# Optimization experiments

Hardware: AMD Instinct MI355X
Metric: run time of the kernel (lower is better)

Reference implementation:

```python
import jax, jax.numpy as jnp
import numpy as np

N, E, G = 50000, 800000, 512
HD, ED, GD, HID = 128, 64, 64, 128  # h_dim, e_dim, g_dim, hid_dim


def _mlp2(x, W1, b1, W2, b2, last_act):
    # Linear -> ReLU -> Linear (-> optional last activation)
    y = jax.nn.relu(x @ W1 + b1) @ W2 + b2
    return last_act(y) if last_act is not None else y


def setup_inputs() -> dict:
    key = jax.random.key(0)
    ks = list(jax.random.split(key, 24))
    ki = iter(ks)

    def p(shape):
        return (jax.random.normal(next(ki), shape, jnp.float32) * 0.02)

    inp = {
        "h": jax.random.normal(next(ki), (N, HD), jnp.float32),
        "e_index": jax.random.randint(next(ki), (2, E), 0, N),
        "e": jax.random.normal(next(ki), (E, ED), jnp.float32),
        "g": jax.random.normal(next(ki), (G, GD), jnp.float32),
        "batch": jnp.sort(jax.random.randint(next(ki), (N,), 0, G)),
        # fc_m: [2*HD+ED+GD, HID, HID], last_activation=relu
        "W_m1": p((2 * HD + ED + GD, HID)), "b_m1": jnp.zeros((HID,), jnp.float32),
        "W_m2": p((HID, HID)), "b_m2": jnp.zeros((HID,), jnp.float32),
        # fc_m_att: [HID, 1], sigmoid
        "W_ma": p((HID, 1)), "b_ma": jnp.zeros((1,), jnp.float32),
        # fc_e: [HID, ED, ED]
        "W_e1": p((HID, ED)), "b_e1": jnp.zeros((ED,), jnp.float32),
        "W_e2": p((ED, ED)), "b_e2": jnp.zeros((ED,), jnp.float32),
        # fc_h: [HD+HID+GD, HD, HD]
        "W_h1": p((HD + HID + GD, HD)), "b_h1": jnp.zeros((HD,), jnp.float32),
        "W_h2": p((HD, HD)), "b_h2": jnp.zeros((HD,), jnp.float32),
        # fc_h_att: [HD, 1]
        "W_ha": p((HD, 1)), "b_ha": jnp.zeros((1,), jnp.float32),
        # fc_g: [GD+HD, GD, GD]
        "W_g1": p((GD + HD, GD)), "b_g1": jnp.zeros((GD,), jnp.float32),
        "W_g2": p((GD, GD)), "b_g2": jnp.zeros((GD,), jnp.float32),
    }
    return inp


def reference(h, e_index, e, g, batch,
              W_m1, b_m1, W_m2, b_m2, W_ma, b_ma,
              W_e1, b_e1, W_e2, b_e2,
              W_h1, b_h1, W_h2, b_h2, W_ha, b_ha,
              W_g1, b_g1, W_g2, b_g2):
    src, dst = e_index[0], e_index[1]
    e_batch = batch[dst]

    # edge message: concat gathered endpoints + edge feat + gathered global
    m_cat = jnp.concatenate([h[src], h[dst], e, g[e_batch]], axis=1)  # [E, 2HD+ED+GD]
    m = jax.nn.relu(jax.nn.relu(m_cat @ W_m1 + b_m1) @ W_m2 + b_m2)   # [E, HID]
    m_att = jax.nn.sigmoid(m @ W_ma + b_ma)                            # [E, 1]

    e_update = _mlp2(m, W_e1, b_e1, W_e2, b_e2, None)                  # [E, ED]
    e_out = jax.nn.relu(e + e_update)

    m_aggr = jax.ops.segment_sum(m_att * m, dst, num_segments=h.shape[0])  # [N, HID]

    h_cat = jnp.concatenate([h, m_aggr, g[batch]], axis=1)             # [N, HD+HID+GD]
    h_update = _mlp2(h_cat, W_h1, b_h1, W_h2, b_h2, None)
    h_out = jax.nn.relu(h + h_update)                                  # [N, HD]
    h_att = h_out @ W_ha + b_ha                                        # [N, 1]

    h_aggr = jax.ops.segment_sum(h_att * h_out, batch, num_segments=g.shape[0])  # [G, HD]

    g_cat = jnp.concatenate([g, h_aggr], axis=1)                       # [G, GD+HD]
    g_update = _mlp2(g_cat, W_g1, b_g1, W_g2, b_g2, None)
    g_out = jax.nn.relu(g + g_update)

    return (h_out, e_out, g_out)
```

## Files before the change

### kernel.cpp

```cpp
#include <hip/hip_runtime.h>
#include <hip/hip_bf16.h>

#define NN 50000
#define NE 800000
#define NG 512
#define HD 128
#define ED 64
#define GD 64
#define HID 128
#define EB 64

typedef __attribute__((ext_vector_type(8))) short short8;
typedef __attribute__((ext_vector_type(4))) short short4v;
typedef __attribute__((ext_vector_type(2))) float f32x2;
typedef __attribute__((ext_vector_type(4))) float f32x4;

__device__ __forceinline__ short f2bf(float f) {
  union { float f; unsigned u; } v; v.f = f;
  unsigned r = v.u + 0x7fffu + ((v.u >> 16) & 1u);
  return (short)(r >> 16);
}

__device__ __forceinline__ float bf2f(short s) {
  union { unsigned u; float f; } v;
  v.u = ((unsigned)(unsigned short)s) << 16;
  return v.f;
}

__device__ __forceinline__ short8 load_a8(const float* p) {
  const f32x4* q = (const f32x4*)p;
  f32x4 x0 = q[0], x1 = q[1];
  short8 r;
  r[0]=f2bf(x0[0]); r[1]=f2bf(x0[1]); r[2]=f2bf(x0[2]); r[3]=f2bf(x0[3]);
  r[4]=f2bf(x1[0]); r[5]=f2bf(x1[1]); r[6]=f2bf(x1[2]); r[7]=f2bf(x1[3]);
  return r;
}

__device__ __forceinline__ int swz(int row, int col, int rowBytes) {
  int b = row * rowBytes + col * 2;
  b ^= (row & 7) << 4;
  return b >> 1;
}

__global__ void pack_kernel(const float* __restrict__ Wm1, const float* __restrict__ Wm2,
                            const float* __restrict__ We1, const float* __restrict__ We2,
                            const float* __restrict__ Wh1, const float* __restrict__ Wh2,
                            short* __restrict__ out) {
  int gid = blockIdx.x * 256 + threadIdx.x;
  if (gid >= 135168) return;
  const float* W; int Ncol, base, idx;
  if (gid < 49152)       { W = Wm1; Ncol = 128; base = 0;      idx = gid; }
  else if (gid < 65536)  { W = Wm2; Ncol = 128; base = 49152;  idx = gid - 49152; }
  else if (gid < 73728)  { W = We1; Ncol = 64;  base = 65536;  idx = gid - 65536; }
  else if (gid < 77824)  { W = We2; Ncol = 64;  base = 73728;  idx = gid - 73728; }
  else if (gid < 118784) { W = Wh1; Ncol = 128; base = 77824;  idx = gid - 77824; }
  else                   { W = Wh2; Ncol = 128; base = 118784; idx = gid - 118784; }
  int k = idx / Ncol, n = idx % Ncol;
  out[base + (k >> 3) * Ncol * 8 + n * 8 + (k & 7)] = f2bf(W[idx]);
}

__global__ void cast_kernel(const float* __restrict__ h, const float* __restrict__ g,
                            const int* __restrict__ ei,
                            short* __restrict__ h_bf, short* __restrict__ g_bf,
                            int* __restrict__ deg) {
  int gid = blockIdx.x * 256 + threadIdx.x;
  const int H4 = NN * HD / 4;
  const int G4 = NG * GD / 4;
  if (gid < H4) {
    f32x4 v = ((const f32x4*)h)[gid];
    short4v r; r[0]=f2bf(v[0]); r[1]=f2bf(v[1]); r[2]=f2bf(v[2]); r[3]=f2bf(v[3]);
    *(short4v*)(h_bf + gid * 4) = r;
  } else if (gid < H4 + G4) {
    int i = gid - H4;
    f32x4 v = ((const f32x4*)g)[i];
    short4v r; r[0]=f2bf(v[0]); r[1]=f2bf(v[1]); r[2]=f2bf(v[2]); r[3]=f2bf(v[3]);
    *(short4v*)(g_bf + i * 4) = r;
  } else if (gid < H4 + G4 + NE) {
    int i = gid - H4 - G4;
    atomicAdd(&deg[ei[NE + i]], 1);
  }
}

__global__ __launch_bounds__(1024) void scan_kernel(int* __restrict__ deg) {
  __shared__ int psum[1024];
  const int CH = 49;
  int t = threadIdx.x;
  int lo = t * CH, hi = lo + CH; if (hi > NN) hi = NN; if (lo > NN) lo = NN;
  int s = 0;
  for (int i = lo; i < hi; ++i) s += deg[i];
  psum[t] = s;
  __syncthreads();
  for (int d = 1; d < 1024; d <<= 1) {
    int v = (t >= d) ? psum[t - d] : 0;
    __syncthreads();
    psum[t] += v;
    __syncthreads();
  }
  int run = (t == 0) ? 0 : psum[t - 1];
  for (int i = lo; i < hi; ++i) { int v = deg[i]; deg[i] = run; run += v; }
}

__global__ void scatter_kernel(const int* __restrict__ ei, int* __restrict__ off,
                               int* __restrict__ elist) {
  int i = blockIdx.x * 256 + threadIdx.x;
  if (i < NE) {
    int d = ei[NE + i];
    int p = atomicAdd(&off[d], 1);
    elist[p] = i;
  }
}

__global__ __launch_bounds__(256) void edge_kernel(
    const short* __restrict__ h_bf, const int* __restrict__ ei,
    const float* __restrict__ e, const short* __restrict__ g_bf,
    const int* __restrict__ batch, const int* __restrict__ elist,
    const short* __restrict__ pWm1, const float* __restrict__ bm1,
    const short* __restrict__ pWm2, const float* __restrict__ bm2,
    const float* __restrict__ Wma, const float* __restrict__ bma,
    const short* __restrict__ pWe1, const float* __restrict__ be1,
    const short* __restrict__ pWe2, const float* __restrict__ be2,
    float* __restrict__ e_out, float* __restrict__ m_aggr) {
  __shared__ short lds_m[EB * 128];
  __shared__ short bufB[2][4096];
  __shared__ float att_s[EB];
  __shared__ int sdst[EB];
  __shared__ int seid[EB];
  short* ebuf = lds_m;

  const int tid = threadIdx.x;
  const int w = tid >> 6;
  const int lane = tid & 63;
  const int row16 = lane & 15;
  const int quad = lane >> 4;

  int nwg = gridDim.x;
  int q = nwg >> 3, rr = nwg & 7;
  int xcd = blockIdx.x & 7;
  int idx = blockIdx.x >> 3;
  int bid = (xcd < rr ? xcd * (q + 1) : rr * (q + 1) + (xcd - rr) * q) + idx;
  const int eb = bid * EB;

#define STAGE(Wp, c, b) do {                                                  \
    const short* _s = (Wp) + (size_t)(c) * 4096;                              \
    short8 _v0 = *(const short8*)(_s + tid * 8);                              \
    short8 _v1 = *(const short8*)(_s + 2048 + tid * 8);                       \
    *(short8*)&bufB[(b)][tid * 8] = _v0;                                      \
    *(short8*)&bufB[(b)][2048 + tid * 8] = _v1;                               \
  } while (0)

  if (tid < EB) {
    int eid = elist[eb + tid];
    seid[tid] = eid;
    sdst[tid] = ei[NE + eid];
  }

  const int eidr = elist[eb + w * 16 + row16];
  const int dstr = ei[NE + eidr];
  const int srcr = ei[eidr];
  const int gbr = batch[dstr];

  const short* seg0 = h_bf + (size_t)srcr * HD;
  const short* seg1 = h_bf + (size_t)dstr * HD;
  const short* seg3 = g_bf + (size_t)gbr * GD;

  short8 ea0, ea1;
  {
    const float* ep = e + (size_t)eidr * ED + quad * 8;
    ea0 = load_a8(ep);
    ea1 = load_a8(ep + 32);
  }

  f32x4 acc[8];
#pragma unroll
  for (int t = 0; t < 8; ++t) acc[t] = (f32x4)0.0f;

  STAGE(pWm1, 0, 0);
  __syncthreads();
#pragma unroll
  for (int c = 0; c < 12; ++c) {
    if (c < 11) STAGE(pWm1, c + 1, (c + 1) & 1);
    else        STAGE(pWm2, 0, 0);
    short8 a;
    if (c < 4)       a = *(const short8*)(seg0 + c * 32 + quad * 8);
    else if (c < 8)  a = *(const short8*)(seg1 + (c - 4) * 32 + quad * 8);
    else if (c == 8) a = ea0;
    else if (c == 9) a = ea1;
    else             a = *(const short8*)(seg3 + (c - 10) * 32 + quad * 8);
    const short* bc = &bufB[c & 1][quad * 1024 + row16 * 8];
#pragma unroll
    for (int t = 0; t < 8; ++t) {
      short8 b = *(const short8*)(bc + t * 128);
      acc[t] = __builtin_amdgcn_mfma_f32_16x16x32_bf16(a, b, acc[t], 0, 0, 0);
    }
    __syncthreads();
  }
#pragma unroll
  for (int t = 0; t < 8; ++t) {
    float b1 = bm1[t * 16 + row16];
#pragma unroll
    for (int r = 0; r < 4; ++r) {
      float y = fmaxf(acc[t][r] + b1, 0.f);
      lds_m[swz(w * 16 + quad * 4 + r, t * 16 + row16, 256)] = f2bf(y);
    }
  }

  f32x4 acc2[8];
#pragma unroll
  for (int t = 0; t < 8; ++t) acc2[t] = (f32x4)0.0f;
#pragma unroll
  for (int c = 0; c < 4; ++c) {
    if (c < 3) STAGE(pWm2, c + 1, (c + 1) & 1);
    short8 a = *(const short8*)&lds_m[swz(w * 16 + row16, c * 32 + quad * 8, 256)];
    const short* bc = &bufB[c & 1][quad * 1024 + row16 * 8];
#pragma unroll
    for (int t = 0; t < 8; ++t) {
      short8 b = *(const short8*)(bc + t * 128);
      acc2[t] = __builtin_amdgcn_mfma_f32_16x16x32_bf16(a, b, acc2[t], 0, 0, 0);
    }
    __syncthreads();
  }

  float p[4] = {0.f, 0.f, 0.f, 0.f};
#pragma unroll
  for (int t = 0; t < 8; ++t) {
    float b2 = bm2[t * 16 + row16];
    float wv = Wma[t * 16 + row16];
#pragma unroll
    for (int r = 0; r < 4; ++r) {
      float y = fmaxf(acc2[t][r] + b2, 0.f);
      lds_m[swz(w * 16 + quad * 4 + r, t * 16 + row16, 256)] = f2bf(y);
      p[r] += y * wv;
    }
  }

#pragma unroll
  for (int s = 1; s < 16; s <<= 1) {
#pragma unroll
    for (int r = 0; r < 4; ++r) p[r] += __shfl_xor(p[r], s, 64);
  }
  {
    float bma0 = bma[0];
    if (row16 == 0) {
#pragma unroll
      for (int r = 0; r < 4; ++r)
        att_s[w * 16 + quad * 4 + r] = 1.f / (1.f + __expf(-(p[r] + bma0)));
    }
  }

  f32x4 acc3[4];
#pragma unroll
  for (int t = 0; t < 4; ++t) acc3[t] = (f32x4)0.0f;
#pragma unroll
  for (int c = 0; c < 4; ++c) {
    short8 a = *(const short8*)&lds_m[swz(w * 16 + row16, c * 32 + quad * 8, 256)];
    const short* bp = pWe1 + (size_t)(c * 4 + quad) * (ED * 8) + row16 * 8;
#pragma unroll
    for (int t = 0; t < 4; ++t) {
      short8 b = *(const short8*)(bp + t * 16 * 8);
      acc3[t] = __builtin_amdgcn_mfma_f32_16x16x32_bf16(a, b, acc3[t], 0, 0, 0);
    }
  }

  __syncthreads();

  {
    int cp = tid & 63;
    int r0 = (tid >> 6) * 16;
    int cur = sdst[r0];
    float s0 = 0.f, s1 = 0.f;
    bool first = true;
#pragma unroll 1
    for (int r = r0; r < r0 + 16; ++r) {
      int d = sdst[r];
      unsigned u = *(const unsigned*)&lds_m[swz(r, cp * 2, 256)];
      float av = att_s[r];
      float v0 = bf2f((short)(u & 0xffffu)) * av;
      float v1 = bf2f((short)(u >> 16)) * av;
      if (d != cur) {
        if (first) {
          atomicAdd(&m_aggr[(size_t)cur * HID + cp * 2], s0);
          atomicAdd(&m_aggr[(size_t)cur * HID + cp * 2 + 1], s1);
        } else {
          f32x2 st; st[0] = s0; st[1] = s1;
          *(f32x2*)&m_aggr[(size_t)cur * HID + cp * 2] = st;
        }
        first = false; cur = d; s0 = v0; s1 = v1;
      } else {
        s0 += v0; s1 += v1;
      }
    }
    atomicAdd(&m_aggr[(size_t)cur * HID + cp * 2], s0);
    atomicAdd(&m_aggr[(size_t)cur * HID + cp * 2 + 1], s1);
  }

  __syncthreads();

#pragma unroll
  for (int t = 0; t < 4; ++t) {
    float b1 = be1[t * 16 + row16];
#pragma unroll
    for (int r = 0; r < 4; ++r) {
      float y = fmaxf(acc3[t][r] + b1, 0.f);
      ebuf[swz(w * 16 + quad * 4 + r, t * 16 + row16, 128)] = f2bf(y);
    }
  }

  f32x4 acc4[4];
#pragma unroll
  for (int t = 0; t < 4; ++t) acc4[t] = (f32x4)0.0f;
#pragma unroll
  for (int c = 0; c < 2; ++c) {
    short8 a = *(const short8*)&ebuf[swz(w * 16 + row16, c * 32 + quad * 8, 128)];
    const short* bp = pWe2 + (size_t)(c * 4 + quad) * (ED * 8) + row16 * 8;
#pragma unroll
    for (int t = 0; t < 4; ++t) {
      short8 b = *(const short8*)(bp + t * 16 * 8);
      acc4[t] = __builtin_amdgcn_mfma_f32_16x16x32_bf16(a, b, acc4[t], 0, 0, 0);
    }
  }

  int eidS[4];
#pragma unroll
  for (int r = 0; r < 4; ++r) eidS[r] = seid[w * 16 + quad * 4 + r];
#pragma unroll
  for (int t = 0; t < 4; ++t) {
    float b2 = be2[t * 16 + row16];
#pragma unroll
    for (int r = 0; r < 4; ++r) {
      int col = t * 16 + row16;
      float res = e[(size_t)eidS[r] * ED + col];
      float v = res + acc4[t][r] + b2;
      e_out[(size_t)eidS[r] * ED + col] = fmaxf(v, 0.f);
    }
  }
#undef STAGE
}

__global__ __launch_bounds__(256) void node_kernel(
    const float* __restrict__ h, const short* __restrict__ h_bf,
    const float* __restrict__ m_aggr, const short* __restrict__ g_bf,
    const int* __restrict__ batch,
    const short* __restrict__ pWh1, const float* __restrict__ bh1,
    const short* __restrict__ pWh2, const float* __restrict__ bh2,
    const float* __restrict__ Wha, const float* __restrict__ bha,
    float* __restrict__ h_out, float* __restrict__ h_aggr) {
  __shared__ short lds_y[4][16 * 128];
  __shared__ int sbat[64];

  const int wave = threadIdx.x >> 6;
  const int lane = threadIdx.x & 63;
  const int row16 = lane & 15;
  const int quad = lane >> 4;
  const int nbase = blockIdx.x * 64 + wave * 16;

  int nA = nbase + row16;
  int nAc = nA < NN ? nA : NN - 1;
  int gbA = batch[nAc];
  if (quad == 0) sbat[wave * 16 + row16] = (nA < NN) ? gbA : -1;

  short8 afr[10];
  {
    const short* s0 = h_bf + (size_t)nAc * HD;
    const float* s1 = m_aggr + (size_t)nAc * HID;
    const short* s2 = g_bf + (size_t)gbA * GD;
#pragma unroll
    for (int c = 0; c < 4; ++c) afr[c] = *(const short8*)(s0 + c * 32 + quad * 8);
#pragma unroll
    for (int c = 0; c < 4; ++c) afr[4 + c] = load_a8(s1 + c * 32 + quad * 8);
    afr[8] = *(const short8*)(s2 + quad * 8);
    afr[9] = *(const short8*)(s2 + 32 + quad * 8);
  }

  f32x4 acc[8];
#pragma unroll
  for (int t = 0; t < 8; ++t) acc[t] = (f32x4)0.0f;
#pragma unroll
  for (int c = 0; c < 10; ++c) {
    const short* bp = pWh1 + (size_t)(c * 4 + quad) * HD * 8 + row16 * 8;
#pragma unroll
    for (int t = 0; t < 8; ++t) {
      short8 b = *(const short8*)(bp + t * 16 * 8);
      acc[t] = __builtin_amdgcn_mfma_f32_16x16x32_bf16(afr[c], b, acc[t], 0, 0, 0);
    }
  }
#pragma unroll
  for (int t = 0; t < 8; ++t) {
    float b1 = bh1[t * 16 + row16];
#pragma unroll
    for (int r = 0; r < 4; ++r) {
      float y = fmaxf(acc[t][r] + b1, 0.f);
      lds_y[wave][swz(quad * 4 + r, t * 16 + row16, 256)] = f2bf(y);
    }
  }

  f32x4 acc2[8];
#pragma unroll
  for (int t = 0; t < 8; ++t) acc2[t] = (f32x4)0.0f;
#pragma unroll
  for (int c = 0; c < 4; ++c) {
    short8 a = *(const short8*)&lds_y[wave][swz(row16, c * 32 + quad * 8, 256)];
    const short* bp = pWh2 + (size_t)(c * 4 + quad) * HD * 8 + row16 * 8;
#pragma unroll
    for (int t = 0; t < 8; ++t) {
      short8 b = *(const short8*)(bp + t * 16 * 8);
      acc2[t] = __builtin_amdgcn_mfma_f32_16x16x32_bf16(a, b, acc2[t], 0, 0, 0);
    }
  }

  float hval[8][4];
  int nS[4];
#pragma unroll
  for (int r = 0; r < 4; ++r) nS[r] = nbase + quad * 4 + r;
#pragma unroll
  for (int t = 0; t < 8; ++t) {
    float b2 = bh2[t * 16 + row16];
#pragma unroll
    for (int r = 0; r < 4; ++r) {
      float v = 0.f;
      if (nS[r] < NN) {
        v = h[(size_t)nS[r] * HD + t * 16 + row16] + acc2[t][r] + b2;
        v = fmaxf(v, 0.f);
        h_out[(size_t)nS[r] * HD + t * 16 + row16] = v;
      }
      hval[t][r] = v;
    }
  }

  float part[4] = {0.f, 0.f, 0.f, 0.f};
#pragma unroll
  for (int t = 0; t < 8; ++t) {
    float w = Wha[t * 16 + row16];
#pragma unroll
    for (int r = 0; r < 4; ++r) part[r] += hval[t][r] * w;
  }
#pragma unroll
  for (int s = 1; s < 16; s <<= 1) {
#pragma unroll
    for (int r = 0; r < 4; ++r) part[r] += __shfl_xor(part[r], s, 64);
  }
  float bha0 = bha[0];
#pragma unroll
  for (int t = 0; t < 8; ++t)
#pragma unroll
    for (int r = 0; r < 4; ++r)
      lds_y[wave][swz(quad * 4 + r, t * 16 + row16, 256)] =
          f2bf((part[r] + bha0) * hval[t][r]);

  __syncthreads();

  {
    int col = threadIdx.x & 127;
    int r0 = (threadIdx.x >> 7) * 32;
    int cur = sbat[r0];
    float sum = 0.f;
    bool first = true;
#pragma unroll 1
    for (int r = r0; r < r0 + 32; ++r) {
      int d = sbat[r];
      float v = bf2f(lds_y[r >> 4][swz(r & 15, col, 256)]);
      if (d != cur) {
        if (cur >= 0) {
          if (first) atomicAdd(&h_aggr[(size_t)cur * HD + col], sum);
          else h_aggr[(size_t)cur * HD + col] = sum;
        }
        first = false; cur = d; sum = v;
      } else {
        sum += v;
      }
    }
    if (cur >= 0) atomicAdd(&h_aggr[(size_t)cur * HD + col], sum);
  }
}

__global__ void g_kernel(const float* __restrict__ g, const float* __restrict__ h_aggr,
                         const float* __restrict__ Wg1, const float* __restrict__ bg1,
                         const float* __restrict__ Wg2, const float* __restrict__ bg2,
                         float* __restrict__ g_out) {
  __shared__ float cat[192];
  __shared__ float y1[64];
  int r = blockIdx.x;
  int t = threadIdx.x;
  cat[t] = g[(size_t)r * GD + t];
  cat[64 + t] = h_aggr[(size_t)r * HD + t];
  cat[128 + t] = h_aggr[(size_t)r * HD + 64 + t];
  __syncthreads();
  float a = bg1[t];
  for (int k = 0; k < 192; ++k) a += cat[k] * Wg1[k * 64 + t];
  y1[t] = fmaxf(a, 0.f);
  __syncthreads();
  float b = bg2[t];
  for (int k = 0; k < 64; ++k) b += y1[k] * Wg2[k * 64 + t];
  float v = g[(size_t)r * GD + t] + b;
  g_out[(size_t)r * GD + t] = fmaxf(v, 0.f);
}

extern "C" void kernel_launch(void* const* d_in, const int* in_sizes, int n_in,
                              void* d_out, int out_size, void* d_ws, size_t ws_size,
                              hipStream_t stream) {
  const float* h = (const float*)d_in[0];
  const int* ei = (const int*)d_in[1];
  const float* e = (const float*)d_in[2];
  const float* g = (const float*)d_in[3];
  const int* batch = (const int*)d_in[4];
  const float* Wm1 = (const float*)d_in[5];
  const float* bm1 = (const float*)d_in[6];
  const float* Wm2 = (const float*)d_in[7];
  const float* bm2 = (const float*)d_in[8];
  const float* Wma = (const float*)d_in[9];
  const float* bma = (const float*)d_in[10];
  const float* We1 = (const float*)d_in[11];
  const float* be1 = (const float*)d_in[12];
  const float* We2 = (const float*)d_in[13];
  const float* be2 = (const float*)d_in[14];
  const float* Wh1 = (const float*)d_in[15];
  const float* bh1 = (const float*)d_in[16];
  const float* Wh2 = (const float*)d_in[17];
  const float* bh2 = (const float*)d_in[18];
  const float* Wha = (const float*)d_in[19];
  const float* bha = (const float*)d_in[20];
  const float* Wg1 = (const float*)d_in[21];
  const float* bg1 = (const float*)d_in[22];
  const float* Wg2 = (const float*)d_in[23];
  const float* bg2 = (const float*)d_in[24];

  float* out = (float*)d_out;
  float* h_out = out;
  float* e_out = out + (size_t)NN * HD;
  float* g_out = e_out + (size_t)NE * ED;

  char* ws = (char*)d_ws;
  float* m_aggr = (float*)ws;
  float* h_aggr = (float*)(ws + 25600000);
  short* packed = (short*)(ws + 25862144);
  int* deg      = (int*)(ws + 26132480);
  int* elist    = (int*)(ws + 26332480);
  short* h_bf   = (short*)(ws + 29532480);
  short* g_bf   = (short*)(ws + 42332480);
  short* pWm1 = packed;
  short* pWm2 = packed + 49152;
  short* pWe1 = packed + 65536;
  short* pWe2 = packed + 73728;
  short* pWh1 = packed + 77824;
  short* pWh2 = packed + 118784;

  hipMemsetAsync(m_aggr, 0, (size_t)NN * HID * 4, stream);
  hipMemsetAsync(h_aggr, 0, (size_t)NG * HD * 4, stream);
  hipMemsetAsync(deg, 0, (size_t)NN * 4, stream);

  pack_kernel<<<(135168 + 255) / 256, 256, 0, stream>>>(Wm1, Wm2, We1, We2, Wh1, Wh2, packed);
  cast_kernel<<<(2408192 + 255) / 256, 256, 0, stream>>>(h, g, ei, h_bf, g_bf, deg);
  scan_kernel<<<1, 1024, 0, stream>>>(deg);
  scatter_kernel<<<(NE + 255) / 256, 256, 0, stream>>>(ei, deg, elist);

  edge_kernel<<<NE / EB, 256, 0, stream>>>(h_bf, ei, e, g_bf, batch, elist,
                                           pWm1, bm1, pWm2, bm2, Wma, bma,
                                           pWe1, be1, pWe2, be2, e_out, m_aggr);

  node_kernel<<<(NN + 63) / 64, 256, 0, stream>>>(h, h_bf, m_aggr, g_bf, batch,
                                                  pWh1, bh1, pWh2, bh2, Wha, bha,
                                                  h_out, h_aggr);

  g_kernel<<<NG, 64, 0, stream>>>(g, h_aggr, Wg1, bg1, Wg2, bg2, g_out);
}
```

Before: 625.5 us.

## Stage node MLP weights through LDS double buffer and fold weight packing into cast kernel

The node kernel now stages Wh1/Wh2 weight chunks cooperatively into a double-buffered LDS area, and each wave reads its B fragments from LDS instead of issuing its own global loads. The A operands are loaded per chunk rather than kept in registers up front. Separately, the weight-packing kernel is merged into the cast kernel to remove one launch. The node kernel gains block-wide barriers and more LDS use, which may lower occupancy.

```diff
diff --git a/kernel.cpp b/kernel.cpp
--- a/kernel.cpp
+++ b/kernel.cpp
@@ -42,27 +42,13 @@
   return b >> 1;
 }
 
-__global__ void pack_kernel(const float* __restrict__ Wm1, const float* __restrict__ Wm2,
+__global__ void cast_kernel(const float* __restrict__ h, const float* __restrict__ g,
+                            const int* __restrict__ ei,
+                            const float* __restrict__ Wm1, const float* __restrict__ Wm2,
                             const float* __restrict__ We1, const float* __restrict__ We2,
                             const float* __restrict__ Wh1, const float* __restrict__ Wh2,
-                            short* __restrict__ out) {
-  int gid = blockIdx.x * 256 + threadIdx.x;
-  if (gid >= 135168) return;
-  const float* W; int Ncol, base, idx;
-  if (gid < 49152)       { W = Wm1; Ncol = 128; base = 0;      idx = gid; }
-  else if (gid < 65536)  { W = Wm2; Ncol = 128; base = 49152;  idx = gid - 49152; }
-  else if (gid < 73728)  { W = We1; Ncol = 64;  base = 65536;  idx = gid - 65536; }
-  else if (gid < 77824)  { W = We2; Ncol = 64;  base = 73728;  idx = gid - 73728; }
-  else if (gid < 118784) { W = Wh1; Ncol = 128; base = 77824;  idx = gid - 77824; }
-  else                   { W = Wh2; Ncol = 128; base = 118784; idx = gid - 118784; }
-  int k = idx / Ncol, n = idx % Ncol;
-  out[base + (k >> 3) * Ncol * 8 + n * 8 + (k & 7)] = f2bf(W[idx]);
-}
-
-__global__ void cast_kernel(const float* __restrict__ h, const float* __restrict__ g,
-                            const int* __restrict__ ei,
                             short* __restrict__ h_bf, short* __restrict__ g_bf,
-                            int* __restrict__ deg) {
+                            int* __restrict__ deg, short* __restrict__ pout) {
   int gid = blockIdx.x * 256 + threadIdx.x;
   const int H4 = NN * HD / 4;
   const int G4 = NG * GD / 4;
@@ -78,6 +64,17 @@
   } else if (gid < H4 + G4 + NE) {
     int i = gid - H4 - G4;
     atomicAdd(&deg[ei[NE + i]], 1);
+  } else if (gid < H4 + G4 + NE + 135168) {
+    int pid = gid - H4 - G4 - NE;
+    const float* W; int Ncol, base, idx;
+    if (pid < 49152)       { W = Wm1; Ncol = 128; base = 0;      idx = pid; }
+    else if (pid < 65536)  { W = Wm2; Ncol = 128; base = 49152;  idx = pid - 49152; }
+    else if (pid < 73728)  { W = We1; Ncol = 64;  base = 65536;  idx = pid - 65536; }
+    else if (pid < 77824)  { W = We2; Ncol = 64;  base = 73728;  idx = pid - 73728; }
+    else if (pid < 118784) { W = Wh1; Ncol = 128; base = 77824;  idx = pid - 77824; }
+    else                   { W = Wh2; Ncol = 128; base = 118784; idx = pid - 118784; }
+    int k = idx / Ncol, n = idx % Ncol;
+    pout[base + (k >> 3) * Ncol * 8 + n * 8 + (k & 7)] = f2bf(W[idx]);
   }
 }
 
@@ -109,6 +106,14 @@
     elist[p] = i;
   }
 }
+
+#define STAGE(Wp, c, b) do {                                                  \
+    const short* _s = (Wp) + (size_t)(c) * 4096;                              \
+    short8 _v0 = *(const short8*)(_s + tid * 8);                              \
+    short8 _v1 = *(const short8*)(_s + 2048 + tid * 8);                       \
+    *(short8*)&bufB[(b)][tid * 8] = _v0;                                      \
+    *(short8*)&bufB[(b)][2048 + tid * 8] = _v1;                               \
+  } while (0)
 
 __global__ __launch_bounds__(256) void edge_kernel(
     const short* __restrict__ h_bf, const int* __restrict__ ei,
@@ -139,14 +144,6 @@
   int idx = blockIdx.x >> 3;
   int bid = (xcd < rr ? xcd * (q + 1) : rr * (q + 1) + (xcd - rr) * q) + idx;
   const int eb = bid * EB;
-
-#define STAGE(Wp, c, b) do {                                                  \
-    const short* _s = (Wp) + (size_t)(c) * 4096;                              \
-    short8 _v0 = *(const short8*)(_s + tid * 8);                              \
-    short8 _v1 = *(const short8*)(_s + 2048 + tid * 8);                       \
-    *(short8*)&bufB[(b)][tid * 8] = _v0;                                      \
-    *(short8*)&bufB[(b)][2048 + tid * 8] = _v1;                               \
-  } while (0)
 
   if (tid < EB) {
     int eid = elist[eb + tid];
@@ -333,7 +330,6 @@
       e_out[(size_t)eidS[r] * ED + col] = fmaxf(v, 0.f);
     }
   }
-#undef STAGE
 }
 
 __global__ __launch_bounds__(256) void node_kernel(
@@ -344,44 +340,56 @@
     const short* __restrict__ pWh2, const float* __restrict__ bh2,
     const float* __restrict__ Wha, const float* __restrict__ bha,
     float* __restrict__ h_out, float* __restrict__ h_aggr) {
-  __shared__ short lds_y[4][16 * 128];
+  __shared__ short lds_y[64 * 128];
+  __shared__ short bufB[2][4096];
   __shared__ int sbat[64];
 
-  const int wave = threadIdx.x >> 6;
-  const int lane = threadIdx.x & 63;
+  const int tid = threadIdx.x;
+  const int w = tid >> 6;
+  const int lane = tid & 63;
   const int row16 = lane & 15;
   const int quad = lane >> 4;
-  const int nbase = blockIdx.x * 64 + wave * 16;
-
-  int nA = nbase + row16;
+  const int nbase = blockIdx.x * 64;
+
+  int nA = nbase + w * 16 + row16;
   int nAc = nA < NN ? nA : NN - 1;
   int gbA = batch[nAc];
-  if (quad == 0) sbat[wave * 16 + row16] = (nA < NN) ? gbA : -1;
-
-  short8 afr[10];
+  if (tid < 64) {
+    int nn = nbase + tid;
+    sbat[tid] = (nn < NN) ? batch[nn] : -1;
+  }
+
+  const short* seg0 = h_bf + (size_t)nAc * HD;
+  const short* seg3 = g_bf + (size_t)gbA * GD;
+
+  short8 ma[4];
   {
-    const short* s0 = h_bf + (size_t)nAc * HD;
-    const float* s1 = m_aggr + (size_t)nAc * HID;
-    const short* s2 = g_bf + (size_t)gbA * GD;
-#pragma unroll
-    for (int c = 0; c < 4; ++c) afr[c] = *(const short8*)(s0 + c * 32 + quad * 8);
-#pragma unroll
-    for (int c = 0; c < 4; ++c) afr[4 + c] = load_a8(s1 + c * 32 + quad * 8);
-    afr[8] = *(const short8*)(s2 + quad * 8);
-    afr[9] = *(const short8*)(s2 + 32 + quad * 8);
+    const float* mp = m_aggr + (size_t)nAc * HID + quad * 8;
+#pragma unroll
+    for (int c = 0; c < 4; ++c) ma[c] = load_a8(mp + c * 32);
   }
 
   f32x4 acc[8];
 #pragma unroll
   for (int t = 0; t < 8; ++t) acc[t] = (f32x4)0.0f;
+
+  STAGE(pWh1, 0, 0);
+  __syncthreads();
 #pragma unroll
   for (int c = 0; c < 10; ++c) {
-    const short* bp = pWh1 + (size_t)(c * 4 + quad) * HD * 8 + row16 * 8;
+    if (c < 9) STAGE(pWh1, c + 1, (c + 1) & 1);
+    else       STAGE(pWh2, 0, 0);
+    short8 a;
+    if (c < 4)      a = *(const short8*)(seg0 + c * 32 + quad * 8);
+    else if (c < 8) a = ma[c - 4];
+    else            a = *(const short8*)(seg3 + (c - 8) * 32 + quad * 8);
+    const short* bc = &bufB[c & 1][quad * 1024 + row16 * 8];
 #pragma unroll
     for (int t = 0; t < 8; ++t) {
-      short8 b = *(const short8*)(bp + t * 16 * 8);
-      acc[t] = __builtin_amdgcn_mfma_f32_16x16x32_bf16(afr[c], b, acc[t], 0, 0, 0);
-    }
+      short8 b = *(const short8*)(bc + t * 128);
+      acc[t] = __builtin_amdgcn_mfma_f32_16x16x32_bf16(a, b, acc[t], 0, 0, 0);
+    }
+    __syncthreads();
   }
 #pragma unroll
   for (int t = 0; t < 8; ++t) {
@@ -389,7 +397,7 @@
 #pragma unroll
     for (int r = 0; r < 4; ++r) {
       float y = fmaxf(acc[t][r] + b1, 0.f);
-      lds_y[wave][swz(quad * 4 + r, t * 16 + row16, 256)] = f2bf(y);
+      lds_y[swz(w * 16 + quad * 4 + r, t * 16 + row16, 256)] = f2bf(y);
     }
   }
 
@@ -398,19 +406,21 @@
   for (int t = 0; t < 8; ++t) acc2[t] = (f32x4)0.0f;
 #pragma unroll
   for (int c = 0; c < 4; ++c) {
-    short8 a = *(const short8*)&lds_y[wave][swz(row16, c * 32 + quad * 8, 256)];
-    const short* bp = pWh2 + (size_t)(c * 4 + quad) * HD * 8 + row16 * 8;
+    if (c < 3) STAGE(pWh2, c + 1, (c + 1) & 1);
+    short8 a = *(const short8*)&lds_y[swz(w * 16 + row16, c * 32 + quad * 8, 256)];
+    const short* bc = &bufB[c & 1][quad * 1024 + row16 * 8];
 #pragma unroll
     for (int t = 0; t < 8; ++t) {
-      short8 b = *(const short8*)(bp + t * 16 * 8);
+      short8 b = *(const short8*)(bc + t * 128);
       acc2[t] = __builtin_amdgcn_mfma_f32_16x16x32_bf16(a, b, acc2[t], 0, 0, 0);
     }
+    __syncthreads();
   }
 
   float hval[8][4];
   int nS[4];
 #pragma unroll
-  for (int r = 0; r < 4; ++r) nS[r] = nbase + quad * 4 + r;
+  for (int r = 0; r < 4; ++r) nS[r] = nbase + w * 16 + quad * 4 + r;
 #pragma unroll
   for (int t = 0; t < 8; ++t) {
     float b2 = bh2[t * 16 + row16];
@@ -429,9 +439,9 @@
   float part[4] = {0.f, 0.f, 0.f, 0.f};
 #pragma unroll
   for (int t = 0; t < 8; ++t) {
-    float w = Wha[t * 16 + row16];
-#pragma unroll
-    for (int r = 0; r < 4; ++r) part[r] += hval[t][r] * w;
+    float wv = Wha[t * 16 + row16];
+#pragma unroll
+    for (int r = 0; r < 4; ++r) part[r] += hval[t][r] * wv;
   }
 #pragma unroll
   for (int s = 1; s < 16; s <<= 1) {
@@ -443,21 +453,21 @@
   for (int t = 0; t < 8; ++t)
 #pragma unroll
     for (int r = 0; r < 4; ++r)
-      lds_y[wave][swz(quad * 4 + r, t * 16 + row16, 256)] =
+      lds_y[swz(w * 16 + quad * 4 + r, t * 16 + row16, 256)] =
           f2bf((part[r] + bha0) * hval[t][r]);
 
   __syncthreads();
 
   {
-    int col = threadIdx.x & 127;
-    int r0 = (threadIdx.x >> 7) * 32;
+    int col = tid & 127;
+    int r0 = (tid >> 7) * 32;
     int cur = sbat[r0];
     float sum = 0.f;
     bool first = true;
 #pragma unroll 1
     for (int r = r0; r < r0 + 32; ++r) {
       int d = sbat[r];
-      float v = bf2f(lds_y[r >> 4][swz(r & 15, col, 256)]);
+      float v = bf2f(lds_y[swz(r, col, 256)]);
       if (d != cur) {
         if (cur >= 0) {
           if (first) atomicAdd(&h_aggr[(size_t)cur * HD + col], sum);
@@ -547,8 +557,8 @@
   hipMemsetAsync(h_aggr, 0, (size_t)NG * HD * 4, stream);
   hipMemsetAsync(deg, 0, (size_t)NN * 4, stream);
 
-  pack_kernel<<<(135168 + 255) / 256, 256, 0, stream>>>(Wm1, Wm2, We1, We2, Wh1, Wh2, packed);
-  cast_kernel<<<(2408192 + 255) / 256, 256, 0, stream>>>(h, g, ei, h_bf, g_bf, deg);
+  cast_kernel<<<(2543360 + 255) / 256, 256, 0, stream>>>(
+      h, g, ei, Wm1, Wm2, We1, We2, Wh1, Wh2, h_bf, g_bf, deg, packed);
   scan_kernel<<<1, 1024, 0, stream>>>(deg);
   scatter_kernel<<<(NE + 255) / 256, 256, 0, stream>>>(ei, deg, elist);
 
```

After: 627.9 us. Within noise of the previous version (+0.4%).
